# Performance work log

Measured on AMD Instinct MI355X. Metric: run time of the kernel, lower is better.

## Reference

```python
import jax, jax.numpy as jnp
import numpy as np

B, H, W, C = 8, 64, 64, 64
DI = 2 * C   # d_inner = ssm_ratio * hidden_dim
N = 1        # ssm_d_state
K = 4        # scan directions
R = 4        # dt_rank = ceil(C/16)
EPS = 1e-5


def _ln(x, w, b):
    mu = x.mean(-1, keepdims=True)
    var = x.var(-1, keepdims=True)
    return (x - mu) / jnp.sqrt(var + EPS) * w + b


def _vss(x, p):
    (norm1_w, norm1_b, in_proj_w, conv_w, x_proj_w, dt_projs_w, dt_projs_b,
     A_logs, Ds, out_norm_w, out_norm_b, out_proj_w, norm2_w, norm2_b,
     fc1_w, fc1_b, fc2_w, fc2_b) = p
    # ---- SS2D branch (forward_type='v2') ----
    h = _ln(x, norm1_w, norm1_b)
    xz = h @ in_proj_w.T                      # (B,H,W,2*DI)
    xc, z = jnp.split(xz, 2, axis=-1)
    z = jax.nn.silu(z)
    xc = xc.transpose(0, 3, 1, 2)             # (B,DI,H,W)
    xc = jax.lax.conv_general_dilated(
        xc, conv_w, (1, 1), [(1, 1), (1, 1)], feature_group_count=DI,
        dimension_numbers=('NCHW', 'OIHW', 'NCHW'))  # depthwise 3x3, no bias
    xc = jax.nn.silu(xc)
    L = H * W
    # CrossScan: row-major, col-major, and their reverses
    x0 = xc.reshape(B, DI, L)
    x1 = xc.transpose(0, 1, 3, 2).reshape(B, DI, L)
    xs = jnp.stack([x0, x1, x0[..., ::-1], x1[..., ::-1]], axis=1)  # (B,K,DI,L)
    x_dbl = jnp.einsum('bkdl,kcd->bkcl', xs, x_proj_w)
    dts, Bs, Cs = x_dbl[:, :, :R], x_dbl[:, :, R:R + N], x_dbl[:, :, R + N:]
    delta = jax.nn.softplus(jnp.einsum('bkrl,kdr->bkdl', dts, dt_projs_w)
                            + dt_projs_b[None, :, :, None])          # (B,K,DI,L)
    A = -jnp.exp(A_logs).reshape(K, DI, N)
    # diagonal linear recurrence h_t = a_t*h_{t-1} + b_t via associative scan
    a = jnp.exp(delta[..., None] * A[None, :, :, None, :])           # (B,K,DI,L,N)
    b = delta[..., None] * Bs.transpose(0, 1, 3, 2)[:, :, None] * xs[..., None]
    def comb(c1, c2):
        a1, b1 = c1
        a2, b2 = c2
        return a1 * a2, b1 * a2 + b2
    _, hst = jax.lax.associative_scan(comb, (a, b), axis=3)          # (B,K,DI,L,N)
    ys = jnp.einsum('bkdln,bknl->bkdl', hst, Cs) \
         + Ds.reshape(K, DI)[None, :, :, None] * xs
    # CrossMerge
    ys = ys[:, :2] + ys[:, 2:, :, ::-1]
    y = ys[:, 0] + ys[:, 1].reshape(B, DI, W, H).transpose(0, 1, 3, 2).reshape(B, DI, L)
    y = y.transpose(0, 2, 1).reshape(B, H, W, DI)
    y = _ln(y, out_norm_w, out_norm_b)
    y = (y * z) @ out_proj_w.T
    x = x + y
    # ---- MLP branch ----
    h2 = _ln(x, norm2_w, norm2_b)
    h2 = jax.nn.gelu(h2 @ fc1_w.T + fc1_b, approximate=False)
    return x + (h2 @ fc2_w.T + fc2_b)


def setup_inputs():
    key = jax.random.key(0)
    ks = jax.random.split(key, 16)
    g = lambda i, shape, s=0.02: jax.random.normal(ks[i], shape, jnp.float32) * s
    return {
        'mag': jax.random.normal(ks[0], (B, H, W, C), jnp.float32),
        'phase': jax.random.normal(ks[1], (B, H, W, C), jnp.float32),
        'norm1_w': jnp.ones((2, C)), 'norm1_b': jnp.zeros((2, C)),
        'in_proj_w': g(2, (2, 2 * DI, C)),
        'conv_w': g(3, (2, DI, 1, 3, 3), 0.1),
        'x_proj_w': g(4, (2, K, R + 2 * N, DI)),
        'dt_projs_w': g(5, (2, K, DI, R), 0.1),
        'dt_projs_b': g(6, (2, K, DI), 0.1),
        'A_logs': g(7, (2, K * DI, N), 1.0),
        'Ds': jnp.ones((2, K * DI)),
        'out_norm_w': jnp.ones((2, DI)), 'out_norm_b': jnp.zeros((2, DI)),
        'out_proj_w': g(8, (2, C, DI)),
        'norm2_w': jnp.ones((2, C)), 'norm2_b': jnp.zeros((2, C)),
        'fc1_w': g(9, (2, 4 * C, C)), 'fc1_b': jnp.zeros((2, 4 * C)),
        'fc2_w': g(10, (2, C, 4 * C)), 'fc2_b': jnp.zeros((2, C)),
    }


def reference(mag, phase, norm1_w, norm1_b, in_proj_w, conv_w, x_proj_w,
              dt_projs_w, dt_projs_b, A_logs, Ds, out_norm_w, out_norm_b,
              out_proj_w, norm2_w, norm2_b, fc1_w, fc1_b, fc2_w, fc2_b):
    params = (norm1_w, norm1_b, in_proj_w, conv_w, x_proj_w, dt_projs_w,
              dt_projs_b, A_logs, Ds, out_norm_w, out_norm_b, out_proj_w,
              norm2_w, norm2_b, fc1_w, fc1_b, fc2_w, fc2_b)
    outs = jax.vmap(_vss)(jnp.stack([mag, phase]), params)  # branch dim = 2
    s = outs[0] + outs[1]
    return (s, s)
```

## Files before the change

### kernel.cpp

```cpp
#include <hip/hip_runtime.h>
#include <math.h>

#define LL   4096
#define DI   128
#define CC   64
#define BB   8
#define KK   4
#define LB   32768
#define NPIX 2097152
#define EPSF 1e-5f

#define OFF_XCIN   ((size_t)0)
#define OFF_XCONV  ((size_t)4194304)
#define OFF_XCONVT ((size_t)8388608)
#define OFF_Z      ((size_t)12582912)
#define OFF_Y      ((size_t)16777216)
#define OFF_YT     ((size_t)20971520)
#define OFF_XDBL   ((size_t)25165824)
#define ISTRIDE    ((size_t)25952256)
#define OFF_YCOMBT OFF_XCIN
#define OFF_XNEW   OFF_YT
#define OFF_SB     OFF_Y

typedef short v8s __attribute__((ext_vector_type(8)));
typedef float v4f __attribute__((ext_vector_type(4)));

__device__ __forceinline__ float fexp_(float x){ return __expf(x); }
__device__ __forceinline__ float silu_(float x){ return __fdividef(x, 1.f+__expf(-x)); }
__device__ __forceinline__ float softplusf_(float x){
  return fmaxf(x,0.f) + __logf(1.f + __expf(-fabsf(x)));
}
__device__ __forceinline__ float geluf_(float x){ return 0.5f*x*(1.f+erff(x*0.70710678118f)); }
__device__ __forceinline__ short bf16_(float x){
  unsigned u = __float_as_uint(x);
  u += 0x7FFF + ((u>>16)&1);
  return (short)(u>>16);
}
__device__ __forceinline__ float bf2f_(short s){
  return __uint_as_float(((unsigned)(unsigned short)s)<<16);
}

#define LD16(dst, ptr) { const float4* p4_=(const float4*)(ptr);                 \
  float4 v0_=p4_[0], v1_=p4_[1], v2_=p4_[2], v3_=p4_[3];                         \
  dst[0]=v0_.x; dst[1]=v0_.y; dst[2]=v0_.z; dst[3]=v0_.w;                        \
  dst[4]=v1_.x; dst[5]=v1_.y; dst[6]=v1_.z; dst[7]=v1_.w;                        \
  dst[8]=v2_.x; dst[9]=v2_.y; dst[10]=v2_.z; dst[11]=v2_.w;                      \
  dst[12]=v3_.x; dst[13]=v3_.y; dst[14]=v3_.z; dst[15]=v3_.w; }
#define LD16H(dst, ptr) { const v8s* p8_=(const v8s*)(ptr);                      \
  v8s a0_=p8_[0], a1_=p8_[1];                                                    \
  _Pragma("unroll") for(int e_=0;e_<8;++e_){ dst[e_]=bf2f_(a0_[e_]);             \
                                             dst[8+e_]=bf2f_(a1_[e_]); } }
#define LD16HR(dst, ptr) { const v8s* p8_=(const v8s*)(ptr);                     \
  v8s a0_=p8_[0], a1_=p8_[1];                                                    \
  _Pragma("unroll") for(int e_=0;e_<8;++e_){ dst[15-e_]=bf2f_(a0_[e_]);          \
                                             dst[7-e_]=bf2f_(a1_[e_]); } }
#define ST16H(ptr, srcv) { v8s o0_, o1_;                                         \
  _Pragma("unroll") for(int e_=0;e_<8;++e_){ o0_[e_]=bf16_(srcv[e_]);            \
                                             o1_[e_]=bf16_(srcv[8+e_]); }        \
  ((v8s*)(ptr))[0]=o0_; ((v8s*)(ptr))[1]=o1_; }

__global__ __launch_bounds__(256) void k1_ln_inproj(
    const float* __restrict__ xmag, const float* __restrict__ xph,
    const float* __restrict__ n1w_, const float* __restrict__ n1b_,
    const float* __restrict__ ipw_, float* __restrict__ ws)
{
  const int i = blockIdx.y;
  const float* xin = i ? xph : xmag;
  const float* n1w = n1w_ + i*CC;
  const float* n1b = n1b_ + i*CC;
  const float* ipw = ipw_ + i*2*DI*CC;
  float* base = ws + (size_t)i*ISTRIDE;
  const int t = threadIdx.x, lane = t & 63;
  const int wv = __builtin_amdgcn_readfirstlane(t >> 6);
  const int m = lane & 15, quad = lane >> 4;
  const int p0 = blockIdx.x*64;
  const int b = p0 >> 12, l0 = p0 & (LL-1);

  __shared__ short hlds[64*72];
  __shared__ short w1lds[128*72];
  __shared__ float outs[128*68];

  {
    float hn[CC];
    const float* xr = xin + (size_t)(p0 + lane)*CC;
    LD16(hn, xr); LD16((hn+16), xr+16); LD16((hn+32), xr+32); LD16((hn+48), xr+48);
    float s1=0.f, s2=0.f;
    #pragma unroll
    for(int c=0;c<CC;++c){ s1 += hn[c]; s2 += hn[c]*hn[c]; }
    const float mu = s1*(1.f/CC);
    const float rs = rsqrtf(s2*(1.f/CC) - mu*mu + EPSF);
    if(wv==0){
      #pragma unroll
      for(int q=0;q<8;++q){
        v8s s;
        #pragma unroll
        for(int e=0;e<8;++e){
          const int c = q*8+e;
          s[e] = bf16_((hn[c]-mu)*rs*n1w[c] + n1b[c]);
        }
        *(v8s*)&hlds[lane*72 + q*8] = s;
      }
    }
  }

  for(int h=0; h<2; ++h){
    if(h) __syncthreads();
    {
      const int jl = t >> 1, hc = (t & 1)*32;
      const float* src = ipw + (size_t)(h*128 + jl)*64 + hc;
      #pragma unroll
      for(int q=0;q<4;++q){
        const float4 fa = ((const float4*)src)[q*2];
        const float4 fb = ((const float4*)src)[q*2+1];
        v8s s;
        s[0]=bf16_(fa.x); s[1]=bf16_(fa.y); s[2]=bf16_(fa.z); s[3]=bf16_(fa.w);
        s[4]=bf16_(fb.x); s[5]=bf16_(fb.y); s[6]=bf16_(fb.z); s[7]=bf16_(fb.w);
        *(v8s*)&w1lds[jl*72 + hc + q*8] = s;
      }
    }
    __syncthreads();
    #pragma unroll 2
    for(int nt=0; nt<8; ++nt){
      v4f acc = (v4f){0.f,0.f,0.f,0.f};
      #pragma unroll
      for(int ks=0; ks<2; ++ks){
        const v8s a = *(const v8s*)&hlds[(wv*16 + m)*72 + ks*32 + quad*8];
        const v8s bb = *(const v8s*)&w1lds[(nt*16 + m)*72 + ks*32 + quad*8];
        acc = __builtin_amdgcn_mfma_f32_16x16x32_bf16(a, bb, acc, 0, 0, 0);
      }
      *(float4*)&outs[(nt*16 + m)*68 + wv*16 + quad*4] =
          make_float4(acc[0], acc[1], acc[2], acc[3]);
    }
    __syncthreads();
    const int jl = t >> 1, hc = (t & 1)*32;
    if(h==0){
      short* xcb = (short*)(base + OFF_XCIN) + (size_t)b*DI*LL + (size_t)jl*LL + l0 + hc;
      const float* so = &outs[jl*68 + hc];
      ST16H(xcb, so);
      ST16H(xcb+16, (so+16));
    } else {
      short* zr = (short*)(base + OFF_Z) + (size_t)jl*LB + p0 + hc;
      float tmp[32];
      #pragma unroll
      for(int e=0;e<32;++e) tmp[e] = silu_(outs[jl*68 + hc + e]);
      ST16H(zr, tmp);
      ST16H(zr+16, (tmp+16));
    }
  }
}

__global__ __launch_bounds__(256) void k2_dwconv(
    const float* __restrict__ cw_, float* __restrict__ ws)
{
  const int i = blockIdx.y;
  const int bd = blockIdx.x;
  const int d = bd & (DI-1);
  const float* cw = cw_ + i*DI*9 + d*9;
  const short* xcin = (const short*)(ws + (size_t)i*ISTRIDE + OFF_XCIN) + (size_t)bd*LL;
  short* xconv  = (short*)(ws + (size_t)i*ISTRIDE + OFF_XCONV ) + (size_t)bd*LL;
  short* xconvT = (short*)(ws + (size_t)i*ISTRIDE + OFF_XCONVT) + (size_t)bd*LL;
  __shared__ float tin[64*65];
  __shared__ float tout[64*65];
  const int t = threadIdx.x;
  float w9[9];
  #pragma unroll
  for(int q=0;q<9;++q) w9[q] = cw[q];
  for(int idx=t; idx<4096; idx+=256)
    tin[(idx>>6)*65 + (idx&63)] = bf2f_(xcin[idx]);
  __syncthreads();
  const int w = t & 63, hb = (t>>6)*16;
  #pragma unroll
  for(int r=0;r<16;++r){
    const int h = hb + r;
    float acc = 0.f;
    #pragma unroll
    for(int dy=0;dy<3;++dy){
      const int hh = h + dy - 1;
      if(hh>=0 && hh<64){
        #pragma unroll
        for(int dx=0;dx<3;++dx){
          const int ww = w + dx - 1;
          if(ww>=0 && ww<64) acc += tin[hh*65+ww]*w9[dy*3+dx];
        }
      }
    }
    const float o = silu_(acc);
    tout[h*65+w] = o;
    xconv[h*64+w] = bf16_(o);
  }
  __syncthreads();
  const int hcol = t & 63, wb = (t>>6)*16;
  #pragma unroll
  for(int r=0;r<16;++r){
    const int wp = wb + r;
    xconvT[wp*64 + hcol] = bf16_(tout[hcol*65 + wp]);
  }
}

__global__ __launch_bounds__(256) void k3a_xproj(
    const float* __restrict__ xpw_, float* __restrict__ ws)
{
  const int i = blockIdx.z;
  const int b = blockIdx.y >> 1;
  const int kp = blockIdx.y & 1;
  const int l = blockIdx.x*256 + threadIdx.x;
  const short* src = (const short*)(ws + (size_t)i*ISTRIDE + (kp? OFF_XCONVT : OFF_XCONV))
                     + (size_t)b*DI*LL;
  const float* xpwF = xpw_ + i*KK*6*DI + kp*6*DI;
  const float* xpwB = xpw_ + i*KK*6*DI + (kp+2)*6*DI;
  float accF[6] = {0,0,0,0,0,0};
  float accB[6] = {0,0,0,0,0,0};
  for(int d=0; d<DI; ++d){
    const float xv = bf2f_(src[(size_t)d*LL + l]);
    #pragma unroll
    for(int c=0;c<6;++c){
      accF[c] += xv * xpwF[c*DI + d];
      accB[c] += xv * xpwB[c*DI + d];
    }
  }
  short* xdF = (short*)(ws + (size_t)i*ISTRIDE + OFF_XDBL) + (size_t)(b*KK+kp  )*6*LL;
  short* xdB = (short*)(ws + (size_t)i*ISTRIDE + OFF_XDBL) + (size_t)(b*KK+kp+2)*6*LL;
  #pragma unroll
  for(int c=0;c<6;++c) xdF[(size_t)c*LL + l] = bf16_(accF[c]);
  #pragma unroll
  for(int c=0;c<6;++c) xdB[(size_t)c*LL + (LL-1-l)] = bf16_(accB[c]);
}

__global__ __launch_bounds__(256,3) void k3b_scan(
    const float* __restrict__ dtw_, const float* __restrict__ dtb_,
    const float* __restrict__ alog_, const float* __restrict__ Ds_,
    float* __restrict__ ws)
{
  const int gid = blockIdx.x;
  const int i = blockIdx.y;
  const int d  = gid & (DI-1);
  const int kp = (gid >> 7) & 1;
  const int b  = gid >> 8;
  const int t = threadIdx.x, lane = t & 63, wv = t >> 6;
  float* base = ws + (size_t)i*ISTRIDE;
  const short* src = (const short*)(base + (kp? OFF_XCONVT : OFF_XCONV)) + (size_t)(b*DI+d)*LL;
  short*       dst = (short*)(base + (kp? OFF_YT : OFF_Y)) + (size_t)(b*DI+d)*LL;
  const short* xdF = (const short*)(base + OFF_XDBL) + (size_t)(b*KK+kp  )*6*LL;
  const short* xdB = (const short*)(base + OFF_XDBL) + (size_t)(b*KK+kp+2)*6*LL;
  const int kdF = kp*DI + d, kdB = (kp+2)*DI + d;
  const float4 wF = ((const float4*)dtw_)[i*KK*DI + kdF];
  const float4 wB = ((const float4*)dtw_)[i*KK*DI + kdB];
  const float biasF = dtb_[i*KK*DI + kdF], biasB = dtb_[i*KK*DI + kdB];
  const float AvF = -fexp_(alog_[i*KK*DI + kdF]);
  const float AvB = -fexp_(alog_[i*KK*DI + kdB]);
  const float Dsum = Ds_[i*KK*DI + kdF] + Ds_[i*KK*DI + kdB];
  const int l0 = t*16;
  const int s0 = LL - 16 - l0;

  float vX[16], aF[16], bF[16], aB[16], bB[16];
  float fA = 1.f, fB = 0.f, gA = 1.f, gB = 0.f;
  LD16H(vX, src + l0);

  {
    float pre[16], r0[16];
    LD16H(r0, xdF + 0*LL + l0);
    #pragma unroll
    for(int j=0;j<16;++j) pre[j] = biasF + wF.x*r0[j];
    LD16H(r0, xdF + 1*LL + l0);
    #pragma unroll
    for(int j=0;j<16;++j) pre[j] += wF.y*r0[j];
    LD16H(r0, xdF + 2*LL + l0);
    #pragma unroll
    for(int j=0;j<16;++j) pre[j] += wF.z*r0[j];
    LD16H(r0, xdF + 3*LL + l0);
    #pragma unroll
    for(int j=0;j<16;++j) pre[j] += wF.w*r0[j];
    LD16H(r0, xdF + 4*LL + l0);
    #pragma unroll
    for(int j=0;j<16;++j){
      const float delta = softplusf_(pre[j]);
      aF[j] = fexp_(delta*AvF);
      bF[j] = delta*r0[j]*vX[j];
      fB = fB*aF[j] + bF[j];
      fA *= aF[j];
    }
  }
  {
    float pre[16], r0[16];
    LD16HR(r0, xdB + 0*LL + s0);
    #pragma unroll
    for(int j=0;j<16;++j) pre[j] = biasB + wB.x*r0[j];
    LD16HR(r0, xdB + 1*LL + s0);
    #pragma unroll
    for(int j=0;j<16;++j) pre[j] += wB.y*r0[j];
    LD16HR(r0, xdB + 2*LL + s0);
    #pragma unroll
    for(int j=0;j<16;++j) pre[j] += wB.z*r0[j];
    LD16HR(r0, xdB + 3*LL + s0);
    #pragma unroll
    for(int j=0;j<16;++j) pre[j] += wB.w*r0[j];
    LD16HR(r0, xdB + 4*LL + s0);
    #pragma unroll
    for(int j=15;j>=0;--j){
      const float delta = softplusf_(pre[j]);
      aB[j] = fexp_(delta*AvB);
      bB[j] = delta*r0[j]*vX[j];
      gB = gB*aB[j] + bB[j];
      gA *= aB[j];
    }
  }

  #pragma unroll
  for(int off=1; off<64; off<<=1){
    const float aL = __shfl_up(fA, off);
    const float bL = __shfl_up(fB, off);
    if(lane >= off){ fB = bL*fA + fB; fA = aL*fA; }
  }
  float pA = __shfl_up(fA, 1), pB = __shfl_up(fB, 1);
  if(lane==0){ pA=1.f; pB=0.f; }
  #pragma unroll
  for(int off=1; off<64; off<<=1){
    const float aR = __shfl_down(gA, off);
    const float bR = __shfl_down(gB, off);
    if(lane + off < 64){ gB = gA*bR + gB; gA = gA*aR; }
  }
  float qA = __shfl_down(gA, 1), qB = __shfl_down(gB, 1);
  if(lane==63){ qA=1.f; qB=0.f; }

  __shared__ float wAg[4], wBg[4], vAg[4], vBg[4];
  if(lane==63){ wAg[wv]=fA; wBg[wv]=fB; }
  if(lane==0){ vAg[wv]=gA; vBg[wv]=gB; }
  __syncthreads();
  float eB=0.f;
  for(int u=0; u<wv; ++u){ eB = wAg[u]*eB + wBg[u]; }
  float rB=0.f;
  for(int u=3; u>wv; --u){ rB = vAg[u]*rB + vBg[u]; }

  float hf = pA*eB + pB;
  float hb = qA*rB + qB;

  float out[16], cc[16];
  LD16H(cc, xdF + 5*LL + l0);
  #pragma unroll
  for(int j=0;j<16;++j){
    hf = aF[j]*hf + bF[j];
    out[j] = hf*cc[j] + Dsum*vX[j];
  }
  LD16HR(cc, xdB + 5*LL + s0);
  #pragma unroll
  for(int j=15;j>=0;--j){
    hb = aB[j]*hb + bB[j];
    out[j] += hb*cc[j];
  }
  ST16H(dst + l0, out);
}

__global__ __launch_bounds__(256) void k3c_combine(float* __restrict__ ws)
{
  const int i = blockIdx.y;
  const int b = blockIdx.x >> 4;
  const int tile = blockIdx.x & 15;
  const int h0 = (tile >> 2) * 16, w0 = (tile & 3) * 16;
  const int t = threadIdx.x;
  float* base = ws + (size_t)i*ISTRIDE;
  const short* y  = (const short*)(base + OFF_Y);
  const short* yT = (const short*)(base + OFF_YT);
  short* ycT = (short*)(base + OFF_YCOMBT);
  __shared__ float ytile[16*16*16];
  __shared__ float ytT[16*16*17];
  const int r0 = t >> 4, c0 = t & 15;
  const int hi = t >> 4, wi = t & 15;
  const int l = (h0 + hi)*64 + (w0 + wi);
  for(int dc=0; dc<8; ++dc){
    #pragma unroll 4
    for(int dd=0; dd<16; ++dd){
      const int d = dc*16 + dd;
      const size_t rb = (size_t)(b*DI + d)*LL;
      ytile[dd*256 + t] = bf2f_(y[rb + (size_t)(h0 + r0)*64 + (w0 + c0)]);
      ytT[dd*272 + r0*17 + c0] = bf2f_(yT[rb + (size_t)(w0 + r0)*64 + (h0 + c0)]);
    }
    __syncthreads();
    #pragma unroll 4
    for(int dd=0; dd<16; ++dd){
      const int d = dc*16 + dd;
      ycT[(size_t)d*LB + b*LL + l] = bf16_(ytile[dd*256 + t] + ytT[dd*272 + wi*17 + hi]);
    }
    __syncthreads();
  }
}

__global__ __launch_bounds__(256) void k4a_proj(
    const float* __restrict__ xmag, const float* __restrict__ xph,
    const float* __restrict__ onw_, const float* __restrict__ onb_,
    const float* __restrict__ opw_, float* __restrict__ ws)
{
  const int i = blockIdx.y;
  const float* xin = i ? xph : xmag;
  const float* onw = onw_ + i*DI;
  const float* onb = onb_ + i*DI;
  const float* opw = opw_ + i*CC*DI;
  float* base = ws + (size_t)i*ISTRIDE;
  const short* ycT = (const short*)(base + OFF_YCOMBT);
  const short* zT  = (const short*)(base + OFF_Z);
  const int t = threadIdx.x, lane = t & 63;
  const int wv = __builtin_amdgcn_readfirstlane(t >> 6);
  const int m = lane & 15, quad = lane >> 4;
  const int p0 = blockIdx.x*64;
  const int p = p0 + lane;

  __shared__ short ynlds[64*136];
  __shared__ short wlds[64*136];
  __shared__ float st[64][9];

  float yv[32];
  float s1=0.f, s2=0.f;
  #pragma unroll 8
  for(int c=0;c<32;++c){
    const float v = bf2f_(ycT[(size_t)(wv*32+c)*LB + p]);
    yv[c]=v; s1+=v; s2+=v*v;
  }
  st[lane][wv*2]=s1; st[lane][wv*2+1]=s2;
  __syncthreads();
  const float S1 = st[lane][0]+st[lane][2]+st[lane][4]+st[lane][6];
  const float S2 = st[lane][1]+st[lane][3]+st[lane][5]+st[lane][7];
  const float mu = S1*(1.f/DI);
  const float rs = rsqrtf(S2*(1.f/DI) - mu*mu + EPSF);
  #pragma unroll
  for(int cq=0;cq<8;++cq){
    short4 s4;
    #pragma unroll
    for(int e=0;e<4;++e){
      const int c = cq*4+e;
      const int d = wv*32 + c;
      ((short*)&s4)[e] = bf16_(((yv[c]-mu)*rs*onw[d] + onb[d]) * bf2f_(zT[(size_t)d*LB + p]));
    }
    *(short4*)&ynlds[lane*136 + wv*32 + cq*4] = s4;
  }
  {
    const int ol = t >> 2, seg = (t & 3)*32;
    const float* src = opw + (size_t)ol*DI + seg;
    #pragma unroll
    for(int q=0;q<4;++q){
      const float4 fa = ((const float4*)src)[q*2];
      const float4 fb = ((const float4*)src)[q*2+1];
      v8s s;
      s[0]=bf16_(fa.x); s[1]=bf16_(fa.y); s[2]=bf16_(fa.z); s[3]=bf16_(fa.w);
      s[4]=bf16_(fb.x); s[5]=bf16_(fb.y); s[6]=bf16_(fb.z); s[7]=bf16_(fb.w);
      *(v8s*)&wlds[ol*136 + seg + q*8] = s;
    }
  }
  __syncthreads();

  v4f accs[4];
  #pragma unroll
  for(int nt=0; nt<4; ++nt){
    v4f acc = (v4f){0.f,0.f,0.f,0.f};
    #pragma unroll
    for(int ks=0; ks<4; ++ks){
      const v8s a = *(const v8s*)&ynlds[(wv*16 + m)*136 + ks*32 + quad*8];
      const v8s b = *(const v8s*)&wlds[(nt*16 + m)*136 + ks*32 + quad*8];
      acc = __builtin_amdgcn_mfma_f32_16x16x32_bf16(a, b, acc, 0, 0, 0);
    }
    accs[nt] = acc;
  }
  short* xnew = (short*)(base + OFF_XNEW);
  #pragma unroll
  for(int nt=0; nt<4; ++nt){
    #pragma unroll
    for(int r=0;r<4;++r){
      const int pp = p0 + wv*16 + quad*4 + r;
      const int o = nt*16 + m;
      xnew[(size_t)pp*CC + o] = bf16_(accs[nt][r] + xin[(size_t)pp*CC + o]);
    }
  }
}

__global__ __launch_bounds__(256) void k4b_mlp(
    const float* __restrict__ n2w_, const float* __restrict__ n2b_,
    const float* __restrict__ f1w_, const float* __restrict__ f1b_,
    const float* __restrict__ f2w_, const float* __restrict__ f2b_,
    float* __restrict__ ws)
{
  const int i = blockIdx.y;
  const float* n2w = n2w_ + i*CC;
  const float* n2b = n2b_ + i*CC;
  const float* f1w = f1w_ + i*256*64;
  const float* f1b = f1b_ + i*256;
  const float* f2w = f2w_ + i*64*256;
  const float* f2b = f2b_ + i*CC;
  float* base = ws + (size_t)i*ISTRIDE;
  const short* xnew = (const short*)(base + OFF_XNEW);
  const int t = threadIdx.x, lane = t & 63;
  const int wv = __builtin_amdgcn_readfirstlane(t >> 6);
  const int m = lane & 15, quad = lane >> 4;
  const int p0 = blockIdx.x*64;

  __shared__ short hlds[64*72];
  __shared__ short w1lds[128*72];
  __shared__ short glds[64*136];
  __shared__ short w2lds[64*136];

  {
    float h2[64];
    const short* xr = xnew + (size_t)(p0 + lane)*CC;
    LD16H(h2, xr); LD16H((h2+16), xr+16); LD16H((h2+32), xr+32); LD16H((h2+48), xr+48);
    float s1=0.f, s2=0.f;
    #pragma unroll
    for(int c=0;c<CC;++c){ s1 += h2[c]; s2 += h2[c]*h2[c]; }
    const float mu = s1*(1.f/CC);
    const float rs = rsqrtf(s2*(1.f/CC) - mu*mu + EPSF);
    if(wv==0){
      #pragma unroll
      for(int q=0;q<8;++q){
        v8s s;
        #pragma unroll
        for(int e=0;e<8;++e){
          const int c = q*8+e;
          s[e] = bf16_((h2[c]-mu)*rs*n2w[c] + n2b[c]);
        }
        *(v8s*)&hlds[lane*72 + q*8] = s;
      }
    }
  }

  v4f acc2[4];
  #pragma unroll
  for(int n=0;n<4;++n) acc2[n] = (v4f){0.f,0.f,0.f,0.f};

  for(int h=0; h<2; ++h){
    if(h) __syncthreads();
    {
      const int jl = t >> 1, hc = (t & 1)*32;
      const float* src = f1w + (size_t)(h*128 + jl)*64 + hc;
      #pragma unroll
      for(int q=0;q<4;++q){
        const float4 fa = ((const float4*)src)[q*2];
        const float4 fb = ((const float4*)src)[q*2+1];
        v8s s;
        s[0]=bf16_(fa.x); s[1]=bf16_(fa.y); s[2]=bf16_(fa.z); s[3]=bf16_(fa.w);
        s[4]=bf16_(fb.x); s[5]=bf16_(fb.y); s[6]=bf16_(fb.z); s[7]=bf16_(fb.w);
        *(v8s*)&w1lds[jl*72 + hc + q*8] = s;
      }
    }
    {
      const int ol = t >> 2, seg = (t & 3)*32;
      const float* src = f2w + (size_t)ol*256 + h*128 + seg;
      #pragma unroll
      for(int q=0;q<4;++q){
        const float4 fa = ((const float4*)src)[q*2];
        const float4 fb = ((const float4*)src)[q*2+1];
        v8s s;
        s[0]=bf16_(fa.x); s[1]=bf16_(fa.y); s[2]=bf16_(fa.z); s[3]=bf16_(fa.w);
        s[4]=bf16_(fb.x); s[5]=bf16_(fb.y); s[6]=bf16_(fb.z); s[7]=bf16_(fb.w);
        *(v8s*)&w2lds[ol*136 + seg + q*8] = s;
      }
    }
    __syncthreads();
    #pragma unroll 2
    for(int nt=0; nt<8; ++nt){
      v4f acc = (v4f){0.f,0.f,0.f,0.f};
      #pragma unroll
      for(int ks=0; ks<2; ++ks){
        const v8s a = *(const v8s*)&hlds[(wv*16 + m)*72 + ks*32 + quad*8];
        const v8s b = *(const v8s*)&w1lds[(nt*16 + m)*72 + ks*32 + quad*8];
        acc = __builtin_amdgcn_mfma_f32_16x16x32_bf16(a, b, acc, 0, 0, 0);
      }
      const float bj = f1b[h*128 + nt*16 + m];
      #pragma unroll
      for(int r=0;r<4;++r){
        glds[(wv*16 + quad*4 + r)*136 + nt*16 + m] = bf16_(geluf_(acc[r] + bj));
      }
    }
    #pragma unroll
    for(int nt=0; nt<4; ++nt){
      v4f acc = acc2[nt];
      #pragma unroll
      for(int ks=0; ks<4; ++ks){
        const v8s a = *(const v8s*)&glds[(wv*16 + m)*136 + ks*32 + quad*8];
        const v8s b = *(const v8s*)&w2lds[(nt*16 + m)*136 + ks*32 + quad*8];
        acc = __builtin_amdgcn_mfma_f32_16x16x32_bf16(a, b, acc, 0, 0, 0);
      }
      acc2[nt] = acc;
    }
  }

  short* sb = (short*)(base + OFF_SB);
  #pragma unroll
  for(int nt=0; nt<4; ++nt){
    const float bo = f2b[nt*16 + m];
    #pragma unroll
    for(int r=0;r<4;++r){
      const int p = p0 + wv*16 + quad*4 + r;
      const int o = nt*16 + m;
      sb[(size_t)p*CC + o] = bf16_(acc2[nt][r] + bo + bf2f_(xnew[(size_t)p*CC + o]));
    }
  }
}

__global__ __launch_bounds__(256) void k5_final(
    const float* __restrict__ ws, float* __restrict__ out)
{
  const int idx = blockIdx.x*256 + threadIdx.x;
  const v8s a = ((const v8s*)(ws + OFF_SB))[idx];
  const v8s b = ((const v8s*)(ws + ISTRIDE + OFF_SB))[idx];
  float4 v0, v1;
  v0.x = bf2f_(a[0])+bf2f_(b[0]); v0.y = bf2f_(a[1])+bf2f_(b[1]);
  v0.z = bf2f_(a[2])+bf2f_(b[2]); v0.w = bf2f_(a[3])+bf2f_(b[3]);
  v1.x = bf2f_(a[4])+bf2f_(b[4]); v1.y = bf2f_(a[5])+bf2f_(b[5]);
  v1.z = bf2f_(a[6])+bf2f_(b[6]); v1.w = bf2f_(a[7])+bf2f_(b[7]);
  ((float4*)out)[idx*2]   = v0;
  ((float4*)out)[idx*2+1] = v1;
  ((float4*)out)[NPIX/4 + idx*2]   = v0;
  ((float4*)out)[NPIX/4 + idx*2+1] = v1;
}

extern "C" void kernel_launch(void* const* d_in, const int* in_sizes, int n_in,
                              void* d_out, int out_size, void* d_ws, size_t ws_size,
                              hipStream_t stream)
{
  const float* mag  = (const float*)d_in[0];
  const float* ph   = (const float*)d_in[1];
  const float* n1w  = (const float*)d_in[2];
  const float* n1b  = (const float*)d_in[3];
  const float* ipw  = (const float*)d_in[4];
  const float* cw   = (const float*)d_in[5];
  const float* xpw  = (const float*)d_in[6];
  const float* dtw  = (const float*)d_in[7];
  const float* dtb  = (const float*)d_in[8];
  const float* alog = (const float*)d_in[9];
  const float* Ds   = (const float*)d_in[10];
  const float* onw  = (const float*)d_in[11];
  const float* onb  = (const float*)d_in[12];
  const float* opw  = (const float*)d_in[13];
  const float* n2w  = (const float*)d_in[14];
  const float* n2b  = (const float*)d_in[15];
  const float* f1w  = (const float*)d_in[16];
  const float* f1b  = (const float*)d_in[17];
  const float* f2w  = (const float*)d_in[18];
  const float* f2b  = (const float*)d_in[19];
  float* ws = (float*)d_ws;
  float* out = (float*)d_out;

  k1_ln_inproj<<<dim3(512,2),  256, 0, stream>>>(mag, ph, n1w, n1b, ipw, ws);
  k2_dwconv   <<<dim3(1024,2), 256, 0, stream>>>(cw, ws);
  k3a_xproj   <<<dim3(16,16,2),256, 0, stream>>>(xpw, ws);
  k3b_scan    <<<dim3(2048,2), 256, 0, stream>>>(dtw, dtb, alog, Ds, ws);
  k3c_combine <<<dim3(128,2),  256, 0, stream>>>(ws);
  k4a_proj    <<<dim3(512,2),  256, 0, stream>>>(mag, ph, onw, onb, opw, ws);
  k4b_mlp     <<<dim3(512,2),  256, 0, stream>>>(n2w, n2b, f1w, f1b, f2w, f2b, ws);
  k5_final    <<<dim3(1024),   256, 0, stream>>>(ws, out);
}
```

Before: 299.4 us.

## Fuse out-projection and MLP kernels, keep residual in LDS; fast erf

```diff
diff --git a/kernel.cpp b/kernel.cpp
--- a/kernel.cpp
+++ b/kernel.cpp
@@ -19,7 +19,6 @@
 #define OFF_XDBL   ((size_t)25165824)
 #define ISTRIDE    ((size_t)25952256)
 #define OFF_YCOMBT OFF_XCIN
-#define OFF_XNEW   OFF_YT
 #define OFF_SB     OFF_Y
 
 typedef short v8s __attribute__((ext_vector_type(8)));
@@ -30,7 +29,15 @@
 __device__ __forceinline__ float softplusf_(float x){
   return fmaxf(x,0.f) + __logf(1.f + __expf(-fabsf(x)));
 }
-__device__ __forceinline__ float geluf_(float x){ return 0.5f*x*(1.f+erff(x*0.70710678118f)); }
+__device__ __forceinline__ float erf_fast_(float x){
+  const float ax = fabsf(x);
+  const float t = __fdividef(1.f, 1.f + 0.3275911f*ax);
+  const float poly = t*(0.254829592f + t*(-0.284496736f + t*(1.421413741f +
+                     t*(-1.453152027f + t*1.061405429f))));
+  const float e = 1.f - poly*__expf(-ax*ax);
+  return copysignf(e, x);
+}
+__device__ __forceinline__ float geluf_(float x){ return 0.5f*x*(1.f+erf_fast_(x*0.70710678118f)); }
 __device__ __forceinline__ short bf16_(float x){
   unsigned u = __float_as_uint(x);
   u += 0x7FFF + ((u>>16)&1);
@@ -384,16 +391,26 @@
   }
 }
 
-__global__ __launch_bounds__(256) void k4a_proj(
+__global__ __launch_bounds__(256) void k4_fused(
     const float* __restrict__ xmag, const float* __restrict__ xph,
     const float* __restrict__ onw_, const float* __restrict__ onb_,
-    const float* __restrict__ opw_, float* __restrict__ ws)
+    const float* __restrict__ opw_,
+    const float* __restrict__ n2w_, const float* __restrict__ n2b_,
+    const float* __restrict__ f1w_, const float* __restrict__ f1b_,
+    const float* __restrict__ f2w_, const float* __restrict__ f2b_,
+    float* __restrict__ ws)
 {
   const int i = blockIdx.y;
   const float* xin = i ? xph : xmag;
   const float* onw = onw_ + i*DI;
   const float* onb = onb_ + i*DI;
   const float* opw = opw_ + i*CC*DI;
+  const float* n2w = n2w_ + i*CC;
+  const float* n2b = n2b_ + i*CC;
+  const float* f1w = f1w_ + i*256*64;
+  const float* f1b = f1b_ + i*256;
+  const float* f2w = f2w_ + i*64*256;
+  const float* f2b = f2b_ + i*CC;
   float* base = ws + (size_t)i*ISTRIDE;
   const short* ycT = (const short*)(base + OFF_YCOMBT);
   const short* zT  = (const short*)(base + OFF_Z);
@@ -403,33 +420,41 @@
   const int p0 = blockIdx.x*64;
   const int p = p0 + lane;
 
-  __shared__ short ynlds[64*136];
-  __shared__ short wlds[64*136];
-  __shared__ float st[64][9];
-
-  float yv[32];
-  float s1=0.f, s2=0.f;
-  #pragma unroll 8
-  for(int c=0;c<32;++c){
-    const float v = bf2f_(ycT[(size_t)(wv*32+c)*LB + p]);
-    yv[c]=v; s1+=v; s2+=v*v;
-  }
-  st[lane][wv*2]=s1; st[lane][wv*2+1]=s2;
-  __syncthreads();
-  const float S1 = st[lane][0]+st[lane][2]+st[lane][4]+st[lane][6];
-  const float S2 = st[lane][1]+st[lane][3]+st[lane][5]+st[lane][7];
-  const float mu = S1*(1.f/DI);
-  const float rs = rsqrtf(S2*(1.f/DI) - mu*mu + EPSF);
-  #pragma unroll
-  for(int cq=0;cq<8;++cq){
-    short4 s4;
-    #pragma unroll
-    for(int e=0;e<4;++e){
-      const int c = cq*4+e;
-      const int d = wv*32 + c;
-      ((short*)&s4)[e] = bf16_(((yv[c]-mu)*rs*onw[d] + onb[d]) * bf2f_(zT[(size_t)d*LB + p]));
-    }
-    *(short4*)&ynlds[lane*136 + wv*32 + cq*4] = s4;
+  __shared__ __align__(16) char pool[71680];
+  short* xnlds = (short*)(pool);
+  short* ynlds = (short*)(pool + 9216);
+  short* wlds  = (short*)(pool + 26624);
+  float (*st)[9] = (float(*)[9])(pool + 44032);
+  short* hlds  = (short*)(pool + 9216);
+  short* w1lds = (short*)(pool + 18432);
+  short* glds  = (short*)(pool + 36864);
+  short* w2lds = (short*)(pool + 54272);
+
+  {
+    float yv[32];
+    float s1=0.f, s2=0.f;
+    #pragma unroll 8
+    for(int c=0;c<32;++c){
+      const float v = bf2f_(ycT[(size_t)(wv*32+c)*LB + p]);
+      yv[c]=v; s1+=v; s2+=v*v;
+    }
+    st[lane][wv*2]=s1; st[lane][wv*2+1]=s2;
+    __syncthreads();
+    const float S1 = st[lane][0]+st[lane][2]+st[lane][4]+st[lane][6];
+    const float S2 = st[lane][1]+st[lane][3]+st[lane][5]+st[lane][7];
+    const float mu = S1*(1.f/DI);
+    const float rs = rsqrtf(S2*(1.f/DI) - mu*mu + EPSF);
+    #pragma unroll
+    for(int cq=0;cq<8;++cq){
+      short4 s4;
+      #pragma unroll
+      for(int e=0;e<4;++e){
+        const int c = cq*4+e;
+        const int d = wv*32 + c;
+        ((short*)&s4)[e] = bf16_(((yv[c]-mu)*rs*onw[d] + onb[d]) * bf2f_(zT[(size_t)d*LB + p]));
+      }
+      *(short4*)&ynlds[lane*136 + wv*32 + cq*4] = s4;
+    }
   }
   {
     const int ol = t >> 2, seg = (t & 3)*32;
@@ -446,7 +471,7 @@
   }
   __syncthreads();
 
-  v4f accs[4];
+  float xnC[16];
   #pragma unroll
   for(int nt=0; nt<4; ++nt){
     v4f acc = (v4f){0.f,0.f,0.f,0.f};
@@ -456,48 +481,26 @@
       const v8s b = *(const v8s*)&wlds[(nt*16 + m)*136 + ks*32 + quad*8];
       acc = __builtin_amdgcn_mfma_f32_16x16x32_bf16(a, b, acc, 0, 0, 0);
     }
-    accs[nt] = acc;
-  }
-  short* xnew = (short*)(base + OFF_XNEW);
-  #pragma unroll
-  for(int nt=0; nt<4; ++nt){
     #pragma unroll
     for(int r=0;r<4;++r){
       const int pp = p0 + wv*16 + quad*4 + r;
       const int o = nt*16 + m;
-      xnew[(size_t)pp*CC + o] = bf16_(accs[nt][r] + xin[(size_t)pp*CC + o]);
-    }
-  }
-}
-
-__global__ __launch_bounds__(256) void k4b_mlp(
-    const float* __restrict__ n2w_, const float* __restrict__ n2b_,
-    const float* __restrict__ f1w_, const float* __restrict__ f1b_,
-    const float* __restrict__ f2w_, const float* __restrict__ f2b_,
-    float* __restrict__ ws)
-{
-  const int i = blockIdx.y;
-  const float* n2w = n2w_ + i*CC;
-  const float* n2b = n2b_ + i*CC;
-  const float* f1w = f1w_ + i*256*64;
-  const float* f1b = f1b_ + i*256;
-  const float* f2w = f2w_ + i*64*256;
-  const float* f2b = f2b_ + i*CC;
-  float* base = ws + (size_t)i*ISTRIDE;
-  const short* xnew = (const short*)(base + OFF_XNEW);
-  const int t = threadIdx.x, lane = t & 63;
-  const int wv = __builtin_amdgcn_readfirstlane(t >> 6);
-  const int m = lane & 15, quad = lane >> 4;
-  const int p0 = blockIdx.x*64;
-
-  __shared__ short hlds[64*72];
-  __shared__ short w1lds[128*72];
-  __shared__ short glds[64*136];
-  __shared__ short w2lds[64*136];
+      xnC[nt*4+r] = acc[r] + xin[(size_t)pp*CC + o];
+    }
+  }
+  __syncthreads();
+  #pragma unroll
+  for(int nt=0; nt<4; ++nt){
+    #pragma unroll
+    for(int r=0;r<4;++r){
+      xnlds[(wv*16 + quad*4 + r)*72 + nt*16 + m] = bf16_(xnC[nt*4+r]);
+    }
+  }
+  __syncthreads();
 
   {
     float h2[64];
-    const short* xr = xnew + (size_t)(p0 + lane)*CC;
+    const short* xr = xnlds + lane*72;
     LD16H(h2, xr); LD16H((h2+16), xr+16); LD16H((h2+32), xr+32); LD16H((h2+48), xr+48);
     float s1=0.f, s2=0.f;
     #pragma unroll
@@ -523,7 +526,7 @@
   for(int n=0;n<4;++n) acc2[n] = (v4f){0.f,0.f,0.f,0.f};
 
   for(int h=0; h<2; ++h){
-    if(h) __syncthreads();
+    __syncthreads();
     {
       const int jl = t >> 1, hc = (t & 1)*32;
       const float* src = f1w + (size_t)(h*128 + jl)*64 + hc;
@@ -585,9 +588,9 @@
     const float bo = f2b[nt*16 + m];
     #pragma unroll
     for(int r=0;r<4;++r){
-      const int p = p0 + wv*16 + quad*4 + r;
+      const int pp = p0 + wv*16 + quad*4 + r;
       const int o = nt*16 + m;
-      sb[(size_t)p*CC + o] = bf16_(acc2[nt][r] + bo + bf2f_(xnew[(size_t)p*CC + o]));
+      sb[(size_t)pp*CC + o] = bf16_(acc2[nt][r] + bo + xnC[nt*4+r]);
     }
   }
 }
@@ -641,7 +644,7 @@
   k3a_xproj   <<<dim3(16,16,2),256, 0, stream>>>(xpw, ws);
   k3b_scan    <<<dim3(2048,2), 256, 0, stream>>>(dtw, dtb, alog, Ds, ws);
   k3c_combine <<<dim3(128,2),  256, 0, stream>>>(ws);
-  k4a_proj    <<<dim3(512,2),  256, 0, stream>>>(mag, ph, onw, onb, opw, ws);
-  k4b_mlp     <<<dim3(512,2),  256, 0, stream>>>(n2w, n2b, f1w, f1b, f2w, f2b, ws);
+  k4_fused    <<<dim3(512,2),  256, 0, stream>>>(mag, ph, onw, onb, opw,
+                                                 n2w, n2b, f1w, f1b, f2w, f2b, ws);
   k5_final    <<<dim3(1024),   256, 0, stream>>>(ws, out);
 }
```

Result: no change. 303.7 us (+1.4%).
